# Kernel tuning notes

Hardware: AMD Instinct MI355X
Metric: run time of the kernel (lower is better)

## Reference

```python
import jax, jax.numpy as jnp
import numpy as np

NHID = 512
T_K, T_Q, B = 256, 128, 8


def setup_inputs() -> dict:
    key = jax.random.key(0)
    k1, k2, k3, k4, k5 = jax.random.split(key, 5)
    query = jax.random.normal(k1, (T_Q, B, NHID), dtype=jnp.float32)
    c_key = jax.random.normal(k2, (T_K, B, NHID), dtype=jnp.float32)
    mask = jax.random.randint(k3, (T_K, B), 0, 2).astype(bool)
    # att_mlp params: Linear(2*nhid, nhid) -> Tanh -> Linear(nhid, 1)
    # stored as [in, out] so y = x @ W + b (torch Linear weight transposed)
    W1 = jax.random.normal(k4, (2 * NHID, NHID), dtype=jnp.float32) / np.sqrt(2 * NHID)
    b1 = jnp.zeros((NHID,), dtype=jnp.float32)
    W2 = jax.random.normal(k5, (NHID, 1), dtype=jnp.float32) / np.sqrt(NHID)
    b2 = jnp.zeros((1,), dtype=jnp.float32)
    return {"query": query, "c_key": c_key, "mask": mask,
            "W1": W1, "b1": b1, "W2": W2, "b2": b2}


def reference(query, c_key, mask, W1, b1, W2, b2):
    H = query.shape[-1]
    # cat([k_expand, q_expand], -1) @ W1 == k @ W1[:H] + q @ W1[H:]
    # (avoids materializing the [T_k, T_q, B, 2H] concat the torch code builds)
    k_proj = jnp.einsum('kbh,hd->kbd', c_key, W1[:H])   # [T_k, B, H]
    q_proj = jnp.einsum('qbh,hd->qbd', query, W1[H:])   # [T_q, B, H]
    h = jnp.tanh(k_proj[:, None, :, :] + q_proj[None, :, :, :] + b1)  # [T_k, T_q, B, H]
    att_score = jnp.einsum('kqbh,ho->kqb', h, W2) + b2[0]             # [T_k, T_q, B]
    att_score = jnp.where(mask[:, None, :], -jnp.inf, att_score)
    att_prob = jax.nn.softmax(att_score, axis=0)                      # softmax over keys
    # c_val defaults to c_key in the original forward
    ant_vec = jnp.einsum('kqb,kbh->qbh', att_prob, c_key)             # [T_q, B, H]
    return ant_vec, att_prob
```

## Files before the change

kernel.cpp:

```cpp
#include <hip/hip_runtime.h>
#include <math.h>

#define NHID 512
#define T_K  256
#define T_Q  128
#define BB   8

constexpr float C2L2E = 2.8853900817779268f;
constexpr float L2E   = 1.4426950408889634f;

__device__ __forceinline__ float fexp2(float x) { return __builtin_amdgcn_exp2f(x); }
__device__ __forceinline__ float frcp(float x)  { return __builtin_amdgcn_rcpf(x); }

typedef __attribute__((ext_vector_type(8))) short bf16x8;
typedef __attribute__((ext_vector_type(4))) float f32x4;

__device__ __forceinline__ unsigned short f2bf(float x) {
    unsigned u = __builtin_bit_cast(unsigned, x);
    unsigned r = (u + 0x7FFFu + ((u >> 16) & 1u)) >> 16;
    return (unsigned short)r;
}
__device__ __forceinline__ float bf2f(unsigned short h) {
    unsigned u = ((unsigned)h) << 16;
    return __builtin_bit_cast(float, u);
}

__global__ __launch_bounds__(256) void convert_w1_kernel(
    const float* __restrict__ W1,
    unsigned short* __restrict__ bt_hi, unsigned short* __restrict__ bt_lo)
{
    const int tb = blockIdx.x;
    const int kt = tb & 15;
    const int nt = tb >> 4;
    __shared__ float tile[64][65];
    const int t  = threadIdx.x;
    const int r  = t >> 2;
    const int c0 = (t & 3) * 16;
    const float* src = W1 + (size_t)(kt * 64 + r) * 512 + nt * 64 + c0;
    #pragma unroll
    for (int j = 0; j < 4; ++j) {
        const float4 v = *(const float4*)&src[j * 4];
        tile[r][c0 + j * 4 + 0] = v.x; tile[r][c0 + j * 4 + 1] = v.y;
        tile[r][c0 + j * 4 + 2] = v.z; tile[r][c0 + j * 4 + 3] = v.w;
    }
    __syncthreads();
    const size_t dst = (size_t)((kt >> 3) * 512 + nt * 64 + r) * 512
                     + (size_t)((kt & 7) * 64 + c0);
    #pragma unroll
    for (int j4 = 0; j4 < 4; ++j4) {
        ushort4 h, l;
        #pragma unroll
        for (int e = 0; e < 4; ++e) {
            const float x = tile[c0 + j4 * 4 + e][r];
            const unsigned short hb = f2bf(x);
            ((unsigned short*)&h)[e] = hb;
            ((unsigned short*)&l)[e] = f2bf(x - bf2f(hb));
        }
        *(ushort4*)&bt_hi[dst + j4 * 4] = h;
        *(ushort4*)&bt_lo[dst + j4 * 4] = l;
    }
}

__global__ __launch_bounds__(256) void proj_kernel(
    const float* __restrict__ qry, const float* __restrict__ ckey,
    const unsigned short* __restrict__ bt_hi, const unsigned short* __restrict__ bt_lo,
    const float* __restrict__ b1,
    uint2* __restrict__ ektq, float* __restrict__ eq)
{
    const int row0 = blockIdx.x * 64;
    const int col0 = blockIdx.y * 64;
    const bool isK = row0 < 2048;
    const int bhalf = isK ? 0 : 512;

    __shared__ __align__(16) unsigned short As_h[64 * 64];
    __shared__ __align__(16) unsigned short As_l[64 * 64];
    __shared__ __align__(16) unsigned short Bs_h[64 * 64];
    __shared__ __align__(16) unsigned short Bs_l[64 * 64];

    const int t    = threadIdx.x;
    const int wave = t >> 6;
    const int lane = t & 63;
    const int wm = (wave & 1) * 32;
    const int wn = (wave >> 1) * 32;

    f32x4 acc[2][2] = {};

    const int sr = t >> 2;
    const int sc = (t & 3) * 16;
    const float* gA = (isK ? ckey + (size_t)(row0 + sr) * 512
                           : qry  + (size_t)(row0 - 2048 + sr) * 512) + sc;
    const unsigned short* gBh = bt_hi + (size_t)(bhalf + col0 + sr) * 512 + sc;
    const unsigned short* gBl = bt_lo + (size_t)(bhalf + col0 + sr) * 512 + sc;
    const int c0c = sc >> 3;
    const int sw0 = ((c0c + 0) ^ (sr & 7)) * 8;
    const int sw1 = ((c0c + 1) ^ (sr & 7)) * 8;

    const int quad = lane >> 4, fr = lane & 15;

    for (int k0 = 0; k0 < 512; k0 += 64) {
        __syncthreads();
        {
            float fa[16];
            *(float4*)&fa[0]  = *(const float4*)&gA[k0 + 0];
            *(float4*)&fa[4]  = *(const float4*)&gA[k0 + 4];
            *(float4*)&fa[8]  = *(const float4*)&gA[k0 + 8];
            *(float4*)&fa[12] = *(const float4*)&gA[k0 + 12];
            union { uint4 v; unsigned short s[8]; } h0, l0, h1, l1;
            #pragma unroll
            for (int e = 0; e < 8; ++e) {
                const unsigned short hb = f2bf(fa[e]);
                h0.s[e] = hb; l0.s[e] = f2bf(fa[e] - bf2f(hb));
            }
            #pragma unroll
            for (int e = 0; e < 8; ++e) {
                const unsigned short hb = f2bf(fa[8 + e]);
                h1.s[e] = hb; l1.s[e] = f2bf(fa[8 + e] - bf2f(hb));
            }
            *(uint4*)&As_h[sr * 64 + sw0] = h0.v; *(uint4*)&As_h[sr * 64 + sw1] = h1.v;
            *(uint4*)&As_l[sr * 64 + sw0] = l0.v; *(uint4*)&As_l[sr * 64 + sw1] = l1.v;
            uint4 v0, v1;
            v0 = *(const uint4*)&gBh[k0];     v1 = *(const uint4*)&gBh[k0 + 8];
            *(uint4*)&Bs_h[sr * 64 + sw0] = v0; *(uint4*)&Bs_h[sr * 64 + sw1] = v1;
            v0 = *(const uint4*)&gBl[k0];     v1 = *(const uint4*)&gBl[k0 + 8];
            *(uint4*)&Bs_l[sr * 64 + sw0] = v0; *(uint4*)&Bs_l[sr * 64 + sw1] = v1;
        }
        __syncthreads();
        #pragma unroll
        for (int ks = 0; ks < 2; ++ks) {
            const int cchunk = ks * 4 + quad;
            bf16x8 afh[2], afl[2], bfh[2], bfl[2];
            #pragma unroll
            for (int mt = 0; mt < 2; ++mt) {
                const int m = wm + mt * 16 + fr;
                afh[mt] = *(const bf16x8*)&As_h[m * 64 + ((cchunk ^ (m & 7)) * 8)];
                afl[mt] = *(const bf16x8*)&As_l[m * 64 + ((cchunk ^ (m & 7)) * 8)];
            }
            #pragma unroll
            for (int nt = 0; nt < 2; ++nt) {
                const int n = wn + nt * 16 + fr;
                bfh[nt] = *(const bf16x8*)&Bs_h[n * 64 + ((cchunk ^ (n & 7)) * 8)];
                bfl[nt] = *(const bf16x8*)&Bs_l[n * 64 + ((cchunk ^ (n & 7)) * 8)];
            }
            #pragma unroll
            for (int mt = 0; mt < 2; ++mt)
                #pragma unroll
                for (int nt = 0; nt < 2; ++nt) {
                    acc[mt][nt] = __builtin_amdgcn_mfma_f32_16x16x32_bf16(afh[mt], bfh[nt], acc[mt][nt], 0, 0, 0);
                    acc[mt][nt] = __builtin_amdgcn_mfma_f32_16x16x32_bf16(afh[mt], bfl[nt], acc[mt][nt], 0, 0, 0);
                    acc[mt][nt] = __builtin_amdgcn_mfma_f32_16x16x32_bf16(afl[mt], bfh[nt], acc[mt][nt], 0, 0, 0);
                }
        }
    }

    #pragma unroll
    for (int nt = 0; nt < 2; ++nt) {
        const int colg = col0 + wn + nt * 16 + fr;
        const float b1v = b1[colg];
        #pragma unroll
        for (int mt = 0; mt < 2; ++mt) {
            #pragma unroll
            for (int i = 0; i < 4; ++i) {
                const int rowg = row0 + wm + mt * 16 + quad * 4 + i;
                const float v = acc[mt][nt][i];
                if (isK) {
                    const float e = fexp2((v + b1v) * C2L2E);
                    const float ep = __shfl_xor(e, 1, 64);
                    unsigned pk = (unsigned)f2bf(e) | ((unsigned)f2bf(ep) << 16);
                    const unsigned pk2 = __shfl_xor(pk, 2, 64);
                    if ((fr & 3) == 0) {
                        const int kidx = rowg >> 3;
                        const int bb   = rowg & 7;
                        const int hq   = colg >> 2;
                        ektq[((size_t)bb * 128 + hq) * 256 + kidx] =
                            make_uint2(pk, pk2);
                    }
                } else {
                    eq[(size_t)(rowg - 2048) * 512 + colg] = fexp2(v * C2L2E);
                }
            }
        }
    }
}

__global__ __launch_bounds__(512) void scoreav_kernel(
    const uint2* __restrict__ ektq, const float* __restrict__ eq,
    const float* __restrict__ W2, const float* __restrict__ b2,
    const int* __restrict__ mask, const float* __restrict__ ckey,
    float* __restrict__ prob_out, float* __restrict__ out_ant)
{
    const int t    = threadIdx.x;
    const int lane = t & 63;
    const int wave = __builtin_amdgcn_readfirstlane(t >> 6);
    const int kk   = t & 255;
    const int half = t >> 8;
    const int q0   = blockIdx.x * 2;
    const int b    = blockIdx.y;

    __shared__ float eq0s[512], eq1s[512], w2s[512];
    __shared__ float rp[2][512];
    __shared__ float ps[2][256];
    __shared__ float pacc[8][2][512];

    eq0s[t] = eq[((size_t)q0 * 8 + b) * 512 + t];
    eq1s[t] = eq[((size_t)(q0 + 1) * 8 + b) * 512 + t];
    w2s[t]  = W2[t];

    const float4 wA = *(const float4*)&W2[lane * 4];
    const float4 wB = *(const float4*)&W2[256 + lane * 4];
    float s2 = wA.x + wA.y + wA.z + wA.w + wB.x + wB.y + wB.z + wB.w;
    #pragma unroll
    for (int m = 32; m; m >>= 1) s2 += __shfl_xor(s2, m, 64);
    const float base = s2 + b2[0];
    __syncthreads();

    const uint2* __restrict__ ekb = ektq + (size_t)b * 128 * 256 + kk;
    float racc0 = 0.0f, racc1 = 0.0f;

    for (int g = 0; g < 8; ++g) {
        uint2 L[8];
        #pragma unroll
        for (int j = 0; j < 8; ++j)
            L[j] = ekb[(size_t)(half * 64 + g * 8 + j) * 256];
        #pragma unroll
        for (int j = 0; j < 8; ++j) {
            const int h = (half * 64 + g * 8 + j) * 4;
            const float ek0 = __builtin_bit_cast(float, L[j].x << 16);
            const float ek1 = __builtin_bit_cast(float, L[j].x & 0xFFFF0000u);
            const float ek2 = __builtin_bit_cast(float, L[j].y << 16);
            const float ek3 = __builtin_bit_cast(float, L[j].y & 0xFFFF0000u);
            const float4 w  = *(const float4*)&w2s[h];
            const float4 e0 = *(const float4*)&eq0s[h];
            const float4 e1 = *(const float4*)&eq1s[h];
            {
                const float a0 = fmaf(ek0, e0.x, 1.0f);
                const float a1 = fmaf(ek1, e0.y, 1.0f);
                const float a2 = fmaf(ek2, e0.z, 1.0f);
                const float a3 = fmaf(ek3, e0.w, 1.0f);
                const float d01 = a0 * a1, d23 = a2 * a3;
                const float n01 = fmaf(w.x, a1, w.y * a0);
                const float n23 = fmaf(w.z, a3, w.w * a2);
                const float N = fmaf(n01, d23, n23 * d01);
                racc0 = fmaf(N, frcp(d01 * d23), racc0);
            }
            {
                const float a0 = fmaf(ek0, e1.x, 1.0f);
                const float a1 = fmaf(ek1, e1.y, 1.0f);
                const float a2 = fmaf(ek2, e1.z, 1.0f);
                const float a3 = fmaf(ek3, e1.w, 1.0f);
                const float d01 = a0 * a1, d23 = a2 * a3;
                const float n01 = fmaf(w.x, a1, w.y * a0);
                const float n23 = fmaf(w.z, a3, w.w * a2);
                const float N = fmaf(n01, d23, n23 * d01);
                racc1 = fmaf(N, frcp(d01 * d23), racc1);
            }
        }
    }
    rp[0][t] = racc0;
    rp[1][t] = racc1;
    __syncthreads();

    if (t < 256) {
        const int msk = mask[t * 8 + b];
        float s0 = base - 2.0f * (rp[0][t] + rp[0][t + 256]);
        float s1 = base - 2.0f * (rp[1][t] + rp[1][t + 256]);
        if (msk) { s0 = -INFINITY; s1 = -INFINITY; }
        ps[0][t] = s0;
        ps[1][t] = s1;
    }
    __syncthreads();

    if (wave < 2) {
        float4 sv = *(const float4*)&ps[wave][lane * 4];
        float m = fmaxf(fmaxf(sv.x, sv.y), fmaxf(sv.z, sv.w));
        #pragma unroll
        for (int d = 32; d; d >>= 1) m = fmaxf(m, __shfl_xor(m, d, 64));
        float4 pv;
        pv.x = fexp2((sv.x - m) * L2E);
        pv.y = fexp2((sv.y - m) * L2E);
        pv.z = fexp2((sv.z - m) * L2E);
        pv.w = fexp2((sv.w - m) * L2E);
        float sum = pv.x + pv.y + pv.z + pv.w;
        #pragma unroll
        for (int d = 32; d; d >>= 1) sum += __shfl_xor(sum, d, 64);
        const float inv = frcp(sum);
        pv.x *= inv; pv.y *= inv; pv.z *= inv; pv.w *= inv;
        *(float4*)&ps[wave][lane * 4] = pv;
        const int qb_idx = (q0 + wave) * 8 + b;
        const int kbase = lane * 4;
        prob_out[(size_t)(kbase + 0) * 1024 + qb_idx] = pv.x;
        prob_out[(size_t)(kbase + 1) * 1024 + qb_idx] = pv.y;
        prob_out[(size_t)(kbase + 2) * 1024 + qb_idx] = pv.z;
        prob_out[(size_t)(kbase + 3) * 1024 + qb_idx] = pv.w;
    }
    __syncthreads();

    {
        const int h0 = lane * 8;
        float4 aL0 = {}, aH0 = {}, aL1 = {}, aH1 = {};
        const int kstart = wave * 32;
        #pragma unroll 4
        for (int ki = 0; ki < 32; ++ki) {
            const int k = kstart + ki;
            const float* ckp = &ckey[((size_t)k * 8 + b) * 512 + h0];
            const float4 c0 = *(const float4*)&ckp[0];
            const float4 c1 = *(const float4*)&ckp[4];
            const float p0 = ps[0][k];
            const float p1 = ps[1][k];
            aL0.x = fmaf(p0, c0.x, aL0.x); aL0.y = fmaf(p0, c0.y, aL0.y);
            aL0.z = fmaf(p0, c0.z, aL0.z); aL0.w = fmaf(p0, c0.w, aL0.w);
            aH0.x = fmaf(p0, c1.x, aH0.x); aH0.y = fmaf(p0, c1.y, aH0.y);
            aH0.z = fmaf(p0, c1.z, aH0.z); aH0.w = fmaf(p0, c1.w, aH0.w);
            aL1.x = fmaf(p1, c0.x, aL1.x); aL1.y = fmaf(p1, c0.y, aL1.y);
            aL1.z = fmaf(p1, c0.z, aL1.z); aL1.w = fmaf(p1, c0.w, aL1.w);
            aH1.x = fmaf(p1, c1.x, aH1.x); aH1.y = fmaf(p1, c1.y, aH1.y);
            aH1.z = fmaf(p1, c1.z, aH1.z); aH1.w = fmaf(p1, c1.w, aH1.w);
        }
        *(float4*)&pacc[wave][0][h0 + 0] = aL0;
        *(float4*)&pacc[wave][0][h0 + 4] = aH0;
        *(float4*)&pacc[wave][1][h0 + 0] = aL1;
        *(float4*)&pacc[wave][1][h0 + 4] = aH1;
    }
    __syncthreads();

    {
        #pragma unroll
        for (int qi = 0; qi < 2; ++qi) {
            float s = 0.f;
            #pragma unroll
            for (int w = 0; w < 8; ++w) s += pacc[w][qi][t];
            out_ant[((size_t)(q0 + qi) * 8 + b) * 512 + t] = s;
        }
    }
}

extern "C" void kernel_launch(void* const* d_in, const int* in_sizes, int n_in,
                              void* d_out, int out_size, void* d_ws, size_t ws_size,
                              hipStream_t stream)
{
    const float* qry  = (const float*)d_in[0];
    const float* ckey = (const float*)d_in[1];
    const int*   mask = (const int*)d_in[2];
    const float* W1   = (const float*)d_in[3];
    const float* b1   = (const float*)d_in[4];
    const float* W2   = (const float*)d_in[5];
    const float* b2   = (const float*)d_in[6];

    float* out_ant  = (float*)d_out;
    float* out_prob = (float*)d_out + T_Q * BB * NHID;

    float* ws = (float*)d_ws;
    uint2* ws_ektq = (uint2*)ws;
    float* ws_eq  = ws + 524288;
    unsigned short* bt_hi = (unsigned short*)(ws + 1048576);
    unsigned short* bt_lo = (unsigned short*)(ws + 1310720);

    convert_w1_kernel<<<dim3(128), 256, 0, stream>>>(W1, bt_hi, bt_lo);
    proj_kernel<<<dim3(48, 8), 256, 0, stream>>>(qry, ckey, bt_hi, bt_lo, b1, ws_ektq, ws_eq);
    scoreav_kernel<<<dim3(64, 8), 512, 0, stream>>>(ws_ektq, ws_eq, W2, b2, mask, ckey,
                                                    out_prob, out_ant);
}
```

Baseline: 117.2 us.

## Prefetch GEMM tiles into registers and read bf16 c_key in the AV pass

```diff
diff --git a/kernel.cpp b/kernel.cpp
--- a/kernel.cpp
+++ b/kernel.cpp
@@ -24,40 +24,66 @@
     unsigned u = ((unsigned)h) << 16;
     return __builtin_bit_cast(float, u);
 }
-
-__global__ __launch_bounds__(256) void convert_w1_kernel(
-    const float* __restrict__ W1,
-    unsigned short* __restrict__ bt_hi, unsigned short* __restrict__ bt_lo)
+__device__ __forceinline__ unsigned packbf(float a, float b) {
+    return (unsigned)f2bf(a) | ((unsigned)f2bf(b) << 16);
+}
+
+__global__ __launch_bounds__(256) void convert_kernel(
+    const float* __restrict__ W1, const float* __restrict__ ckey,
+    unsigned short* __restrict__ bt_hi, unsigned short* __restrict__ bt_lo,
+    unsigned int* __restrict__ ckp)
 {
-    const int tb = blockIdx.x;
-    const int kt = tb & 15;
-    const int nt = tb >> 4;
-    __shared__ float tile[64][65];
-    const int t  = threadIdx.x;
-    const int r  = t >> 2;
-    const int c0 = (t & 3) * 16;
-    const float* src = W1 + (size_t)(kt * 64 + r) * 512 + nt * 64 + c0;
-    #pragma unroll
-    for (int j = 0; j < 4; ++j) {
-        const float4 v = *(const float4*)&src[j * 4];
-        tile[r][c0 + j * 4 + 0] = v.x; tile[r][c0 + j * 4 + 1] = v.y;
-        tile[r][c0 + j * 4 + 2] = v.z; tile[r][c0 + j * 4 + 3] = v.w;
-    }
-    __syncthreads();
-    const size_t dst = (size_t)((kt >> 3) * 512 + nt * 64 + r) * 512
-                     + (size_t)((kt & 7) * 64 + c0);
-    #pragma unroll
-    for (int j4 = 0; j4 < 4; ++j4) {
-        ushort4 h, l;
-        #pragma unroll
-        for (int e = 0; e < 4; ++e) {
-            const float x = tile[c0 + j4 * 4 + e][r];
-            const unsigned short hb = f2bf(x);
-            ((unsigned short*)&h)[e] = hb;
-            ((unsigned short*)&l)[e] = f2bf(x - bf2f(hb));
-        }
-        *(ushort4*)&bt_hi[dst + j4 * 4] = h;
-        *(ushort4*)&bt_lo[dst + j4 * 4] = l;
+    const int bid = blockIdx.x;
+    const int t   = threadIdx.x;
+    if (bid < 128) {
+        const int kt = bid & 15;
+        const int nt = bid >> 4;
+        __shared__ float tile[64][65];
+        const int r  = t >> 2;
+        const int c0 = (t & 3) * 16;
+        const float* src = W1 + (size_t)(kt * 64 + r) * 512 + nt * 64 + c0;
+        #pragma unroll
+        for (int j = 0; j < 4; ++j) {
+            const float4 v = *(const float4*)&src[j * 4];
+            tile[r][c0 + j * 4 + 0] = v.x; tile[r][c0 + j * 4 + 1] = v.y;
+            tile[r][c0 + j * 4 + 2] = v.z; tile[r][c0 + j * 4 + 3] = v.w;
+        }
+        __syncthreads();
+        const size_t dst = (size_t)((kt >> 3) * 512 + nt * 64 + r) * 512
+                         + (size_t)((kt & 7) * 64 + c0);
+        #pragma unroll
+        for (int j4 = 0; j4 < 4; ++j4) {
+            ushort4 h, l;
+            #pragma unroll
+            for (int e = 0; e < 4; ++e) {
+                const float x = tile[c0 + j4 * 4 + e][r];
+                const unsigned short hb = f2bf(x);
+                ((unsigned short*)&h)[e] = hb;
+                ((unsigned short*)&l)[e] = f2bf(x - bf2f(hb));
+            }
+            *(ushort4*)&bt_hi[dst + j4 * 4] = h;
+            *(ushort4*)&bt_lo[dst + j4 * 4] = l;
+        }
+    } else {
+        const int cb = bid - 128;
+        const int b  = cb >> 5;
+        const int kt = cb & 31;
+        const int kloc = t >> 5;
+        const int g    = t & 31;
+        const int k = kt * 8 + kloc;
+        const float* src = ckey + ((size_t)k * 8 + b) * 512 + g * 16;
+        const float4 v0 = *(const float4*)&src[0];
+        const float4 v1 = *(const float4*)&src[4];
+        const float4 v2 = *(const float4*)&src[8];
+        const float4 v3 = *(const float4*)&src[12];
+        uint4 o0, o1;
+        o0.x = packbf(v0.x, v0.y); o0.y = packbf(v0.z, v0.w);
+        o0.z = packbf(v1.x, v1.y); o0.w = packbf(v1.z, v1.w);
+        o1.x = packbf(v2.x, v2.y); o1.y = packbf(v2.z, v2.w);
+        o1.z = packbf(v3.x, v3.y); o1.w = packbf(v3.z, v3.w);
+        unsigned int* dst = ckp + ((size_t)b * 256 + k) * 256 + g * 8;
+        *(uint4*)&dst[0] = o0;
+        *(uint4*)&dst[4] = o1;
     }
 }
 
@@ -97,34 +123,44 @@
 
     const int quad = lane >> 4, fr = lane & 15;
 
+    float4 pa0 = *(const float4*)&gA[0];
+    float4 pa1 = *(const float4*)&gA[4];
+    float4 pa2 = *(const float4*)&gA[8];
+    float4 pa3 = *(const float4*)&gA[12];
+    uint4  pbh0 = *(const uint4*)&gBh[0], pbh1 = *(const uint4*)&gBh[8];
+    uint4  pbl0 = *(const uint4*)&gBl[0], pbl1 = *(const uint4*)&gBl[8];
+
     for (int k0 = 0; k0 < 512; k0 += 64) {
+        float fa[16];
+        *(float4*)&fa[0] = pa0; *(float4*)&fa[4] = pa1;
+        *(float4*)&fa[8] = pa2; *(float4*)&fa[12] = pa3;
+        union { uint4 v; unsigned short s[8]; } h0, l0, h1, l1;
+        #pragma unroll
+        for (int e = 0; e < 8; ++e) {
+            const unsigned short hb = f2bf(fa[e]);
+            h0.s[e] = hb; l0.s[e] = f2bf(fa[e] - bf2f(hb));
+        }
+        #pragma unroll
+        for (int e = 0; e < 8; ++e) {
+            const unsigned short hb = f2bf(fa[8 + e]);
+            h1.s[e] = hb; l1.s[e] = f2bf(fa[8 + e] - bf2f(hb));
+        }
         __syncthreads();
-        {
-            float fa[16];
-            *(float4*)&fa[0]  = *(const float4*)&gA[k0 + 0];
-            *(float4*)&fa[4]  = *(const float4*)&gA[k0 + 4];
-            *(float4*)&fa[8]  = *(const float4*)&gA[k0 + 8];
-            *(float4*)&fa[12] = *(const float4*)&gA[k0 + 12];
-            union { uint4 v; unsigned short s[8]; } h0, l0, h1, l1;
-            #pragma unroll
-            for (int e = 0; e < 8; ++e) {
-                const unsigned short hb = f2bf(fa[e]);
-                h0.s[e] = hb; l0.s[e] = f2bf(fa[e] - bf2f(hb));
-            }
-            #pragma unroll
-            for (int e = 0; e < 8; ++e) {
-                const unsigned short hb = f2bf(fa[8 + e]);
-                h1.s[e] = hb; l1.s[e] = f2bf(fa[8 + e] - bf2f(hb));
-            }
-            *(uint4*)&As_h[sr * 64 + sw0] = h0.v; *(uint4*)&As_h[sr * 64 + sw1] = h1.v;
-            *(uint4*)&As_l[sr * 64 + sw0] = l0.v; *(uint4*)&As_l[sr * 64 + sw1] = l1.v;
-            uint4 v0, v1;
-            v0 = *(const uint4*)&gBh[k0];     v1 = *(const uint4*)&gBh[k0 + 8];
-            *(uint4*)&Bs_h[sr * 64 + sw0] = v0; *(uint4*)&Bs_h[sr * 64 + sw1] = v1;
-            v0 = *(const uint4*)&gBl[k0];     v1 = *(const uint4*)&gBl[k0 + 8];
-            *(uint4*)&Bs_l[sr * 64 + sw0] = v0; *(uint4*)&Bs_l[sr * 64 + sw1] = v1;
-        }
+        *(uint4*)&As_h[sr * 64 + sw0] = h0.v; *(uint4*)&As_h[sr * 64 + sw1] = h1.v;
+        *(uint4*)&As_l[sr * 64 + sw0] = l0.v; *(uint4*)&As_l[sr * 64 + sw1] = l1.v;
+        *(uint4*)&Bs_h[sr * 64 + sw0] = pbh0; *(uint4*)&Bs_h[sr * 64 + sw1] = pbh1;
+        *(uint4*)&Bs_l[sr * 64 + sw0] = pbl0; *(uint4*)&Bs_l[sr * 64 + sw1] = pbl1;
         __syncthreads();
+
+        if (k0 + 64 < 512) {
+            pa0 = *(const float4*)&gA[k0 + 64];
+            pa1 = *(const float4*)&gA[k0 + 68];
+            pa2 = *(const float4*)&gA[k0 + 72];
+            pa3 = *(const float4*)&gA[k0 + 76];
+            pbh0 = *(const uint4*)&gBh[k0 + 64]; pbh1 = *(const uint4*)&gBh[k0 + 72];
+            pbl0 = *(const uint4*)&gBl[k0 + 64]; pbl1 = *(const uint4*)&gBl[k0 + 72];
+        }
+
         #pragma unroll
         for (int ks = 0; ks < 2; ++ks) {
             const int cchunk = ks * 4 + quad;
@@ -165,7 +201,9 @@
                 if (isK) {
                     const float e = fexp2((v + b1v) * C2L2E);
                     const float ep = __shfl_xor(e, 1, 64);
-                    unsigned pk = (unsigned)f2bf(e) | ((unsigned)f2bf(ep) << 16);
+                    unsigned pk = packbf(e, ep);
+                    pk = ((fr & 1) == 0) ? pk
+                       : (unsigned)f2bf(ep) | ((unsigned)f2bf(e) << 16);
                     const unsigned pk2 = __shfl_xor(pk, 2, 64);
                     if ((fr & 3) == 0) {
                         const int kidx = rowg >> 3;
@@ -185,7 +223,7 @@
 __global__ __launch_bounds__(512) void scoreav_kernel(
     const uint2* __restrict__ ektq, const float* __restrict__ eq,
     const float* __restrict__ W2, const float* __restrict__ b2,
-    const int* __restrict__ mask, const float* __restrict__ ckey,
+    const int* __restrict__ mask, const unsigned int* __restrict__ ckp,
     float* __restrict__ prob_out, float* __restrict__ out_ant)
 {
     const int t    = threadIdx.x;
@@ -301,9 +339,16 @@
         #pragma unroll 4
         for (int ki = 0; ki < 32; ++ki) {
             const int k = kstart + ki;
-            const float* ckp = &ckey[((size_t)k * 8 + b) * 512 + h0];
-            const float4 c0 = *(const float4*)&ckp[0];
-            const float4 c1 = *(const float4*)&ckp[4];
+            const uint4 U = *(const uint4*)&ckp[((size_t)b * 256 + k) * 256 + lane * 4];
+            float4 c0, c1;
+            c0.x = __builtin_bit_cast(float, U.x << 16);
+            c0.y = __builtin_bit_cast(float, U.x & 0xFFFF0000u);
+            c0.z = __builtin_bit_cast(float, U.y << 16);
+            c0.w = __builtin_bit_cast(float, U.y & 0xFFFF0000u);
+            c1.x = __builtin_bit_cast(float, U.z << 16);
+            c1.y = __builtin_bit_cast(float, U.z & 0xFFFF0000u);
+            c1.z = __builtin_bit_cast(float, U.w << 16);
+            c1.w = __builtin_bit_cast(float, U.w & 0xFFFF0000u);
             const float p0 = ps[0][k];
             const float p1 = ps[1][k];
             aL0.x = fmaf(p0, c0.x, aL0.x); aL0.y = fmaf(p0, c0.y, aL0.y);
@@ -353,9 +398,10 @@
     float* ws_eq  = ws + 524288;
     unsigned short* bt_hi = (unsigned short*)(ws + 1048576);
     unsigned short* bt_lo = (unsigned short*)(ws + 1310720);
-
-    convert_w1_kernel<<<dim3(128), 256, 0, stream>>>(W1, bt_hi, bt_lo);
+    unsigned int* ws_ckp  = (unsigned int*)(ws + 1572864);
+
+    convert_kernel<<<dim3(384), 256, 0, stream>>>(W1, ckey, bt_hi, bt_lo, ws_ckp);
     proj_kernel<<<dim3(48, 8), 256, 0, stream>>>(qry, ckey, bt_hi, bt_lo, b1, ws_ektq, ws_eq);
-    scoreav_kernel<<<dim3(64, 8), 512, 0, stream>>>(ws_ektq, ws_eq, W2, b2, mask, ckey,
+    scoreav_kernel<<<dim3(64, 8), 512, 0, stream>>>(ws_ektq, ws_eq, W2, b2, mask, ws_ckp,
                                                     out_prob, out_ant);
 }
```

Measured after the change: 113.3 us. 3.3% less time.
